# Kernel tuning notes

Hardware: AMD Instinct MI355X
Metric: run time of the kernel (lower is better)

## Reference

```python
import jax, jax.numpy as jnp
import numpy as np

# Module hyperparameters (init_kwargs)
N_CLASSES = 21
RADIUS = 5
SIZE = (256, 256)
SIGMA_DIST = 4.0
SIGMA_FEAT = 1.0
B, C = 8, 32


def _offsets(radius):
    """Integer (dy, dx) offsets with Euclidean distance < radius (includes (0,0))."""
    offs = []
    r = int(radius)
    for dy in range(-r + 1, r):
        for dx in range(-r + 1, r):
            if dy * dy + dx * dx < radius * radius:
                offs.append((dy, dx))
    return offs


OFFSETS = _offsets(RADIUS)  # 69 offsets for radius=5


def setup_inputs() -> dict:
    key = jax.random.key(0)
    k1, k2 = jax.random.split(key)
    H, W = SIZE
    classification = jax.random.uniform(k1, (B, N_CLASSES, H, W), dtype=jnp.float32)
    features = jax.random.normal(k2, (B, C, H, W), dtype=jnp.float32)
    return {"classification": classification, "features": features}


def reference(classification, features):
    # classification: [B, K, H, W] soft assignments S
    # features:       [B, C, H, W]
    Bb, K, H, W = classification.shape
    inv_sd2 = 1.0 / (SIGMA_DIST * SIGMA_DIST)
    inv_sf2 = 1.0 / (SIGMA_FEAT * SIGMA_FEAT)

    hs = jnp.arange(H)
    ws = jnp.arange(W)

    WS = jnp.zeros_like(classification)           # (W @ S), [B, K, H, W]
    degree = jnp.zeros((Bb, H, W), classification.dtype)

    # Loop over the small fixed set of neighbor offsets (69 for radius=5).
    for dy, dx in OFFSETS:
        f_nb = jnp.roll(features, (-dy, -dx), axis=(2, 3))
        s_nb = jnp.roll(classification, (-dy, -dx), axis=(2, 3))
        # mask out wrap-around: neighbor (h+dy, w+dx) must be in-bounds
        valid_h = (hs + dy >= 0) & (hs + dy < H)
        valid_w = (ws + dx >= 0) & (ws + dx < W)
        mask = (valid_h[:, None] & valid_w[None, :]).astype(classification.dtype)
        # Gaussian affinity: distance kernel * feature kernel
        feat_d2 = ((features - f_nb) ** 2).sum(axis=1)        # [B, H, W]
        w = jnp.exp(-(dy * dy + dx * dx) * inv_sd2 - feat_d2 * inv_sf2) * mask
        WS = WS + w[:, None] * s_nb
        degree = degree + w

    # numerator   = S^T W S : [B, K, K]
    # denominator = d^T S   : [B, K]
    num = jnp.einsum('bkhw,bjhw->bkj', classification, WS)
    den = jnp.einsum('bhw,bkhw->bk', degree, classification)
    return (num / den[:, None, :]).sum()
```

## Files before the change

### kernel.cpp

```cpp
#include <hip/hip_runtime.h>

#define HH 256
#define WW 256
#define HWPX 65536
#define BB 8
#define KK 21
#define CC 32

typedef _Float16 half2v __attribute__((ext_vector_type(2)));
union F4H { float4 f4; half2v h[4]; };

__global__ __launch_bounds__(256) void prep(const float* __restrict__ cls,
                                            const float* __restrict__ feat,
                                            float4* __restrict__ fpk,
                                            float2* __restrict__ TN) {
    const int tid = blockIdx.x * 256 + threadIdx.x;
    const int b = tid >> 16;
    const int p = tid & (HWPX - 1);

    const float* cbase = cls + (size_t)b * KK * HWPX + p;
    float T = 0.f;
#pragma unroll
    for (int k = 0; k < KK; ++k) T += cbase[(size_t)k * HWPX];

    const float* src = feat + (size_t)b * CC * HWPX + p;
    float nq = 0.f;
#pragma unroll
    for (int j = 0; j < 4; ++j) {
        F4H u;
#pragma unroll
        for (int k = 0; k < 4; ++k) {
            float a  = src[(size_t)(j * 8 + 2 * k) * HWPX];
            float b2 = src[(size_t)(j * 8 + 2 * k + 1) * HWPX];
            u.h[k] = __builtin_bit_cast(half2v, __builtin_amdgcn_cvt_pkrtz(a, b2));
            nq = __builtin_amdgcn_fdot2(u.h[k], u.h[k], nq, false);
        }
        fpk[(size_t)j * (BB * HWPX) + tid] = u.f4;
    }
    TN[tid] = make_float2(T, nq);
}

__global__ __launch_bounds__(256) void affinity4(const float4* __restrict__ fpk,
                                                 const float2* __restrict__ TN,
                                                 float* __restrict__ V,
                                                 float* __restrict__ deg) {
    const int L  = blockIdx.x;
    const int b  = L & 7;
    const int t  = L >> 3;
    const int by = t & 15;
    const int bx = (t >> 4) & 3;
    const int half = t >> 6;
    const int lane = threadIdx.x & 63;
    const int wid  = threadIdx.x >> 6;
    const int gx  = bx * 64 + lane;
    const int gy0 = by * 16 + wid * 4;

    const size_t bofs = (size_t)b * HWPX;
    const float4* fb0 = fpk + bofs;
    const float4* fb1 = fpk + (size_t)1 * BB * HWPX + bofs;
    const float4* fb2 = fpk + (size_t)2 * BB * HWPX + bofs;
    const float4* fb3 = fpk + (size_t)3 * BB * HWPX + bofs;
    const float2* tnb = TN + bofs;

    F4H fp[4][4];
    float np_[4];
#pragma unroll
    for (int py = 0; py < 4; ++py) {
        const int pp = ((gy0 + py) << 8) | gx;
        fp[py][0].f4 = fb0[pp];
        fp[py][1].f4 = fb1[pp];
        fp[py][2].f4 = fb2[pp];
        fp[py][3].f4 = fb3[pp];
        np_[py] = tnb[pp].y;
    }

    float degacc[4] = {0.f, 0.f, 0.f, 0.f};
    float vacc[4]   = {0.f, 0.f, 0.f, 0.f};

    const int dy_lo = half * 6;
    const int dy_hi = dy_lo + 6;

#pragma unroll 1
    for (int dyi = dy_lo; dyi < dy_hi; ++dyi) {
        const int ny = gy0 + dyi - 4;
        if ((unsigned)ny >= HH) continue;
        const int rowq = ny << 8;

        int dy2[4];
        float base[4];
#pragma unroll
        for (int py = 0; py < 4; ++py) {
            const int d = dyi - 4 - py;
            dy2[py] = d * d;
            base[py] = fmaf(-0.03125f, (float)dy2[py], -0.5f * np_[py]);
        }
        const int mind = min(min(dy2[0], dy2[1]), min(dy2[2], dy2[3]));

#pragma unroll 3
        for (int dxi = 0; dxi < 9; ++dxi) {
            const int dx = dxi - 4;
            const int dx2 = dx * dx;
            if (mind + dx2 >= 25) continue;

            const int gx2 = gx + dx;
            const bool vx = (unsigned)gx2 < WW;
            const int q = rowq | min(max(gx2, 0), WW - 1);

            F4H nb0, nb1, nb2, nb3;
            nb0.f4 = fb0[q];
            nb1.f4 = fb1[q];
            nb2.f4 = fb2[q];
            nb3.f4 = fb3[q];
            const float2 tq = tnb[q];
            const float cdx = (float)dx2 * -0.03125f;

#pragma unroll
            for (int py = 0; py < 4; ++py) {
                if (dy2[py] + dx2 < 25) {
                    float acc = fmaf(-0.5f, tq.y, base[py] + cdx);
#pragma unroll
                    for (int k = 0; k < 4; ++k) {
                        acc = __builtin_amdgcn_fdot2(fp[py][0].h[k], nb0.h[k], acc, false);
                        acc = __builtin_amdgcn_fdot2(fp[py][1].h[k], nb1.h[k], acc, false);
                        acc = __builtin_amdgcn_fdot2(fp[py][2].h[k], nb2.h[k], acc, false);
                        acc = __builtin_amdgcn_fdot2(fp[py][3].h[k], nb3.h[k], acc, false);
                    }
                    float w = __builtin_exp2f(acc * 2.8853900817779268f);
                    w = vx ? w : 0.f;
                    degacc[py] += w;
                    vacc[py] = fmaf(w, tq.x, vacc[py]);
                }
            }
        }
    }

    float* Vh = V   + (size_t)half * (BB * HWPX);
    float* Dh = deg + (size_t)half * (BB * HWPX);
#pragma unroll
    for (int py = 0; py < 4; ++py) {
        const size_t o = bofs + ((size_t)(gy0 + py) << 8) + gx;
        Vh[o] = vacc[py];
        Dh[o] = degacc[py];
    }
}

__global__ __launch_bounds__(256) void reduce_bj(const float* __restrict__ cls,
                                                 const float* __restrict__ V,
                                                 const float* __restrict__ deg,
                                                 float* __restrict__ numer,
                                                 float* __restrict__ denom) {
    __shared__ float smN[4][22], smD[4][22];
    const int b = blockIdx.y;
    const int p4 = (blockIdx.x * 256 + threadIdx.x) * 4;

    const float* clsb = cls + (size_t)b * KK * HWPX;
    const float* Vb = V + (size_t)b * HWPX;
    const float* Db = deg + (size_t)b * HWPX;
    const float4 va = *(const float4*)(Vb + p4);
    const float4 vb = *(const float4*)(Vb + (size_t)BB * HWPX + p4);
    const float4 da = *(const float4*)(Db + p4);
    const float4 db = *(const float4*)(Db + (size_t)BB * HWPX + p4);
    const float4 v4 = make_float4(va.x + vb.x, va.y + vb.y, va.z + vb.z, va.w + vb.w);
    const float4 d4 = make_float4(da.x + db.x, da.y + db.y, da.z + db.z, da.w + db.w);

    float accN[KK], accD[KK];
#pragma unroll
    for (int j = 0; j < KK; ++j) {
        float4 s4 = *(const float4*)(clsb + (size_t)j * HWPX + p4);
        float n = s4.x * v4.x;  n = fmaf(s4.y, v4.y, n);
        n = fmaf(s4.z, v4.z, n); n = fmaf(s4.w, v4.w, n);
        float d = s4.x * d4.x;  d = fmaf(s4.y, d4.y, d);
        d = fmaf(s4.z, d4.z, d); d = fmaf(s4.w, d4.w, d);
        accN[j] = n; accD[j] = d;
    }

    const int wid = threadIdx.x >> 6;
#pragma unroll
    for (int j = 0; j < KK; ++j) {
        float n = accN[j], d = accD[j];
#pragma unroll
        for (int off = 32; off > 0; off >>= 1) {
            n += __shfl_down(n, off);
            d += __shfl_down(d, off);
        }
        if ((threadIdx.x & 63) == 0) { smN[wid][j] = n; smD[wid][j] = d; }
    }
    __syncthreads();
    if (threadIdx.x < 2 * KK) {
        int half = threadIdx.x / KK;
        int j = threadIdx.x - half * KK;
        float acc = half ? (smD[0][j] + smD[1][j] + smD[2][j] + smD[3][j])
                         : (smN[0][j] + smN[1][j] + smN[2][j] + smN[3][j]);
        float* dst = half ? denom : numer;
        atomicAdd(&dst[b * KK + j], acc);
    }
}

__global__ __launch_bounds__(256) void finalize(const float* __restrict__ numer,
                                                const float* __restrict__ denom,
                                                float* __restrict__ out) {
    __shared__ float sm[4];
    int i = threadIdx.x;
    float r = 0.f;
    if (i < BB * KK) r = numer[i] / denom[i];
#pragma unroll
    for (int off = 32; off > 0; off >>= 1) r += __shfl_down(r, off);
    if ((i & 63) == 0) sm[i >> 6] = r;
    __syncthreads();
    if (i == 0) out[0] = sm[0] + sm[1] + sm[2] + sm[3];
}

extern "C" void kernel_launch(void* const* d_in, const int* in_sizes, int n_in,
                              void* d_out, int out_size, void* d_ws, size_t ws_size,
                              hipStream_t stream) {
    const float* cls  = (const float*)d_in[0];
    const float* feat = (const float*)d_in[1];
    float* out = (float*)d_out;

    const size_t BHW = (size_t)BB * HWPX;
    float4* fpk  = (float4*)d_ws;
    float2* TN   = (float2*)((char*)d_ws + BHW * 64);
    float*  V    = (float*)((char*)TN + BHW * 8);
    float*  deg  = V + 2 * BHW;
    float*  numer = deg + 2 * BHW;
    float*  denom = numer + BB * KK;

    (void)hipMemsetAsync(numer, 0, 2 * BB * KK * sizeof(float), stream);
    prep<<<dim3((BB * HWPX) / 256), dim3(256), 0, stream>>>(cls, feat, fpk, TN);
    affinity4<<<dim3(1024), dim3(256), 0, stream>>>(fpk, TN, V, deg);
    reduce_bj<<<dim3(HWPX / 1024, BB), dim3(256), 0, stream>>>(cls, V, deg, numer, denom);
    finalize<<<dim3(1), dim3(256), 0, stream>>>(numer, denom, out);
}
```

Baseline: 200.9 us.

## Pack per-pixel features and stats into interleaved 80-byte records

```diff
diff --git a/kernel.cpp b/kernel.cpp
--- a/kernel.cpp
+++ b/kernel.cpp
@@ -6,14 +6,14 @@
 #define BB 8
 #define KK 21
 #define CC 32
+#define RECB 80
 
 typedef _Float16 half2v __attribute__((ext_vector_type(2)));
 union F4H { float4 f4; half2v h[4]; };
 
 __global__ __launch_bounds__(256) void prep(const float* __restrict__ cls,
                                             const float* __restrict__ feat,
-                                            float4* __restrict__ fpk,
-                                            float2* __restrict__ TN) {
+                                            char* __restrict__ rec) {
     const int tid = blockIdx.x * 256 + threadIdx.x;
     const int b = tid >> 16;
     const int p = tid & (HWPX - 1);
@@ -24,6 +24,7 @@
     for (int k = 0; k < KK; ++k) T += cbase[(size_t)k * HWPX];
 
     const float* src = feat + (size_t)b * CC * HWPX + p;
+    char* r = rec + (size_t)tid * RECB;
     float nq = 0.f;
 #pragma unroll
     for (int j = 0; j < 4; ++j) {
@@ -35,13 +36,12 @@
             u.h[k] = __builtin_bit_cast(half2v, __builtin_amdgcn_cvt_pkrtz(a, b2));
             nq = __builtin_amdgcn_fdot2(u.h[k], u.h[k], nq, false);
         }
-        fpk[(size_t)j * (BB * HWPX) + tid] = u.f4;
-    }
-    TN[tid] = make_float2(T, nq);
-}
-
-__global__ __launch_bounds__(256) void affinity4(const float4* __restrict__ fpk,
-                                                 const float2* __restrict__ TN,
+        *(float4*)(r + j * 16) = u.f4;
+    }
+    *(float2*)(r + 64) = make_float2(T, nq);
+}
+
+__global__ __launch_bounds__(256) void affinity4(const char* __restrict__ rec,
                                                  float* __restrict__ V,
                                                  float* __restrict__ deg) {
     const int L  = blockIdx.x;
@@ -55,23 +55,19 @@
     const int gx  = bx * 64 + lane;
     const int gy0 = by * 16 + wid * 4;
 
-    const size_t bofs = (size_t)b * HWPX;
-    const float4* fb0 = fpk + bofs;
-    const float4* fb1 = fpk + (size_t)1 * BB * HWPX + bofs;
-    const float4* fb2 = fpk + (size_t)2 * BB * HWPX + bofs;
-    const float4* fb3 = fpk + (size_t)3 * BB * HWPX + bofs;
-    const float2* tnb = TN + bofs;
+    const char* rb = rec + (size_t)b * HWPX * RECB;
 
     F4H fp[4][4];
     float np_[4];
 #pragma unroll
     for (int py = 0; py < 4; ++py) {
         const int pp = ((gy0 + py) << 8) | gx;
-        fp[py][0].f4 = fb0[pp];
-        fp[py][1].f4 = fb1[pp];
-        fp[py][2].f4 = fb2[pp];
-        fp[py][3].f4 = fb3[pp];
-        np_[py] = tnb[pp].y;
+        const char* rp = rb + (size_t)pp * RECB;
+        fp[py][0].f4 = *(const float4*)(rp);
+        fp[py][1].f4 = *(const float4*)(rp + 16);
+        fp[py][2].f4 = *(const float4*)(rp + 32);
+        fp[py][3].f4 = *(const float4*)(rp + 48);
+        np_[py] = *(const float*)(rp + 68);
     }
 
     float degacc[4] = {0.f, 0.f, 0.f, 0.f};
@@ -84,7 +80,7 @@
     for (int dyi = dy_lo; dyi < dy_hi; ++dyi) {
         const int ny = gy0 + dyi - 4;
         if ((unsigned)ny >= HH) continue;
-        const int rowq = ny << 8;
+        const char* rowbase = rb + (size_t)(ny << 8) * RECB;
 
         int dy2[4];
         float base[4];
@@ -104,14 +100,15 @@
 
             const int gx2 = gx + dx;
             const bool vx = (unsigned)gx2 < WW;
-            const int q = rowq | min(max(gx2, 0), WW - 1);
+            const int qx = min(max(gx2, 0), WW - 1);
+            const char* rq = rowbase + (size_t)qx * RECB;
 
             F4H nb0, nb1, nb2, nb3;
-            nb0.f4 = fb0[q];
-            nb1.f4 = fb1[q];
-            nb2.f4 = fb2[q];
-            nb3.f4 = fb3[q];
-            const float2 tq = tnb[q];
+            nb0.f4 = *(const float4*)(rq);
+            nb1.f4 = *(const float4*)(rq + 16);
+            nb2.f4 = *(const float4*)(rq + 32);
+            nb3.f4 = *(const float4*)(rq + 48);
+            const float2 tq = *(const float2*)(rq + 64);
             const float cdx = (float)dx2 * -0.03125f;
 
 #pragma unroll
@@ -136,6 +133,7 @@
 
     float* Vh = V   + (size_t)half * (BB * HWPX);
     float* Dh = deg + (size_t)half * (BB * HWPX);
+    const size_t bofs = (size_t)b * HWPX;
 #pragma unroll
     for (int py = 0; py < 4; ++py) {
         const size_t o = bofs + ((size_t)(gy0 + py) << 8) + gx;
@@ -151,39 +149,31 @@
                                                  float* __restrict__ denom) {
     __shared__ float smN[4][22], smD[4][22];
     const int b = blockIdx.y;
-    const int p4 = (blockIdx.x * 256 + threadIdx.x) * 4;
-
-    const float* clsb = cls + (size_t)b * KK * HWPX;
-    const float* Vb = V + (size_t)b * HWPX;
-    const float* Db = deg + (size_t)b * HWPX;
-    const float4 va = *(const float4*)(Vb + p4);
-    const float4 vb = *(const float4*)(Vb + (size_t)BB * HWPX + p4);
-    const float4 da = *(const float4*)(Db + p4);
-    const float4 db = *(const float4*)(Db + (size_t)BB * HWPX + p4);
-    const float4 v4 = make_float4(va.x + vb.x, va.y + vb.y, va.z + vb.z, va.w + vb.w);
-    const float4 d4 = make_float4(da.x + db.x, da.y + db.y, da.z + db.z, da.w + db.w);
+    const int p = blockIdx.x * 256 + threadIdx.x;
+    const size_t bp = (size_t)b * HWPX + p;
+
+    const float v = V[bp] + V[(size_t)BB * HWPX + bp];
+    const float d = deg[bp] + deg[(size_t)BB * HWPX + bp];
+    const float* clsb = cls + (size_t)b * KK * HWPX + p;
 
     float accN[KK], accD[KK];
 #pragma unroll
     for (int j = 0; j < KK; ++j) {
-        float4 s4 = *(const float4*)(clsb + (size_t)j * HWPX + p4);
-        float n = s4.x * v4.x;  n = fmaf(s4.y, v4.y, n);
-        n = fmaf(s4.z, v4.z, n); n = fmaf(s4.w, v4.w, n);
-        float d = s4.x * d4.x;  d = fmaf(s4.y, d4.y, d);
-        d = fmaf(s4.z, d4.z, d); d = fmaf(s4.w, d4.w, d);
-        accN[j] = n; accD[j] = d;
+        const float s = clsb[(size_t)j * HWPX];
+        accN[j] = s * v;
+        accD[j] = s * d;
     }
 
     const int wid = threadIdx.x >> 6;
 #pragma unroll
     for (int j = 0; j < KK; ++j) {
-        float n = accN[j], d = accD[j];
+        float n = accN[j], dd = accD[j];
 #pragma unroll
         for (int off = 32; off > 0; off >>= 1) {
-            n += __shfl_down(n, off);
-            d += __shfl_down(d, off);
-        }
-        if ((threadIdx.x & 63) == 0) { smN[wid][j] = n; smD[wid][j] = d; }
+            n  += __shfl_down(n, off);
+            dd += __shfl_down(dd, off);
+        }
+        if ((threadIdx.x & 63) == 0) { smN[wid][j] = n; smD[wid][j] = dd; }
     }
     __syncthreads();
     if (threadIdx.x < 2 * KK) {
@@ -218,16 +208,15 @@
     float* out = (float*)d_out;
 
     const size_t BHW = (size_t)BB * HWPX;
-    float4* fpk  = (float4*)d_ws;
-    float2* TN   = (float2*)((char*)d_ws + BHW * 64);
-    float*  V    = (float*)((char*)TN + BHW * 8);
-    float*  deg  = V + 2 * BHW;
-    float*  numer = deg + 2 * BHW;
-    float*  denom = numer + BB * KK;
+    char*  rc   = (char*)d_ws;
+    float* V    = (float*)(rc + BHW * RECB);
+    float* dg   = V + 2 * BHW;
+    float* numer = dg + 2 * BHW;
+    float* denom = numer + BB * KK;
 
     (void)hipMemsetAsync(numer, 0, 2 * BB * KK * sizeof(float), stream);
-    prep<<<dim3((BB * HWPX) / 256), dim3(256), 0, stream>>>(cls, feat, fpk, TN);
-    affinity4<<<dim3(1024), dim3(256), 0, stream>>>(fpk, TN, V, deg);
-    reduce_bj<<<dim3(HWPX / 1024, BB), dim3(256), 0, stream>>>(cls, V, deg, numer, denom);
+    prep<<<dim3((BB * HWPX) / 256), dim3(256), 0, stream>>>(cls, feat, rc);
+    affinity4<<<dim3(1024), dim3(256), 0, stream>>>(rc, V, dg);
+    reduce_bj<<<dim3(HWPX / 256, BB), dim3(256), 0, stream>>>(cls, V, dg, numer, denom);
     finalize<<<dim3(1), dim3(256), 0, stream>>>(numer, denom, out);
 }
```

Result: slower. 225.7 us (+12.3%).

## Fuse class reduction into affinity kernel and split dot-product accumulator chains

Applied to the files above, without the earlier changes.

```diff
diff --git a/kernel.cpp b/kernel.cpp
--- a/kernel.cpp
+++ b/kernel.cpp
@@ -40,10 +40,12 @@
     TN[tid] = make_float2(T, nq);
 }
 
-__global__ __launch_bounds__(256) void affinity4(const float4* __restrict__ fpk,
-                                                 const float2* __restrict__ TN,
-                                                 float* __restrict__ V,
-                                                 float* __restrict__ deg) {
+__global__ __launch_bounds__(256, 4) void affinity4(const float4* __restrict__ fpk,
+                                                    const float2* __restrict__ TN,
+                                                    const float* __restrict__ cls,
+                                                    float* __restrict__ numer,
+                                                    float* __restrict__ denom) {
+    __shared__ float smN[4][22], smD[4][22];
     const int L  = blockIdx.x;
     const int b  = L & 7;
     const int t  = L >> 3;
@@ -117,14 +119,16 @@
 #pragma unroll
             for (int py = 0; py < 4; ++py) {
                 if (dy2[py] + dx2 < 25) {
-                    float acc = fmaf(-0.5f, tq.y, base[py] + cdx);
+                    float c0 = fmaf(-0.5f, tq.y, base[py] + cdx);
+                    float c1 = 0.f, c2 = 0.f, c3 = 0.f;
 #pragma unroll
                     for (int k = 0; k < 4; ++k) {
-                        acc = __builtin_amdgcn_fdot2(fp[py][0].h[k], nb0.h[k], acc, false);
-                        acc = __builtin_amdgcn_fdot2(fp[py][1].h[k], nb1.h[k], acc, false);
-                        acc = __builtin_amdgcn_fdot2(fp[py][2].h[k], nb2.h[k], acc, false);
-                        acc = __builtin_amdgcn_fdot2(fp[py][3].h[k], nb3.h[k], acc, false);
+                        c0 = __builtin_amdgcn_fdot2(fp[py][0].h[k], nb0.h[k], c0, false);
+                        c1 = __builtin_amdgcn_fdot2(fp[py][1].h[k], nb1.h[k], c1, false);
+                        c2 = __builtin_amdgcn_fdot2(fp[py][2].h[k], nb2.h[k], c2, false);
+                        c3 = __builtin_amdgcn_fdot2(fp[py][3].h[k], nb3.h[k], c3, false);
                     }
+                    const float acc = (c0 + c1) + (c2 + c3);
                     float w = __builtin_exp2f(acc * 2.8853900817779268f);
                     w = vx ? w : 0.f;
                     degacc[py] += w;
@@ -134,65 +138,40 @@
         }
     }
 
-    float* Vh = V   + (size_t)half * (BB * HWPX);
-    float* Dh = deg + (size_t)half * (BB * HWPX);
-#pragma unroll
-    for (int py = 0; py < 4; ++py) {
-        const size_t o = bofs + ((size_t)(gy0 + py) << 8) + gx;
-        Vh[o] = vacc[py];
-        Dh[o] = degacc[py];
-    }
-}
-
-__global__ __launch_bounds__(256) void reduce_bj(const float* __restrict__ cls,
-                                                 const float* __restrict__ V,
-                                                 const float* __restrict__ deg,
-                                                 float* __restrict__ numer,
-                                                 float* __restrict__ denom) {
-    __shared__ float smN[4][22], smD[4][22];
-    const int b = blockIdx.y;
-    const int p4 = (blockIdx.x * 256 + threadIdx.x) * 4;
-
     const float* clsb = cls + (size_t)b * KK * HWPX;
-    const float* Vb = V + (size_t)b * HWPX;
-    const float* Db = deg + (size_t)b * HWPX;
-    const float4 va = *(const float4*)(Vb + p4);
-    const float4 vb = *(const float4*)(Vb + (size_t)BB * HWPX + p4);
-    const float4 da = *(const float4*)(Db + p4);
-    const float4 db = *(const float4*)(Db + (size_t)BB * HWPX + p4);
-    const float4 v4 = make_float4(va.x + vb.x, va.y + vb.y, va.z + vb.z, va.w + vb.w);
-    const float4 d4 = make_float4(da.x + db.x, da.y + db.y, da.z + db.z, da.w + db.w);
-
-    float accN[KK], accD[KK];
-#pragma unroll
-    for (int j = 0; j < KK; ++j) {
-        float4 s4 = *(const float4*)(clsb + (size_t)j * HWPX + p4);
-        float n = s4.x * v4.x;  n = fmaf(s4.y, v4.y, n);
-        n = fmaf(s4.z, v4.z, n); n = fmaf(s4.w, v4.w, n);
-        float d = s4.x * d4.x;  d = fmaf(s4.y, d4.y, d);
-        d = fmaf(s4.z, d4.z, d); d = fmaf(s4.w, d4.w, d);
-        accN[j] = n; accD[j] = d;
-    }
-
-    const int wid = threadIdx.x >> 6;
-#pragma unroll
-    for (int j = 0; j < KK; ++j) {
-        float n = accN[j], d = accD[j];
-#pragma unroll
-        for (int off = 32; off > 0; off >>= 1) {
-            n += __shfl_down(n, off);
-            d += __shfl_down(d, off);
-        }
-        if ((threadIdx.x & 63) == 0) { smN[wid][j] = n; smD[wid][j] = d; }
+#pragma unroll 1
+    for (int jc = 0; jc < 3; ++jc) {
+        float accN[7], accD[7];
+#pragma unroll
+        for (int jj = 0; jj < 7; ++jj) {
+            const float* cj = clsb + (size_t)(jc * 7 + jj) * HWPX;
+            float n = 0.f, d = 0.f;
+#pragma unroll
+            for (int py = 0; py < 4; ++py) {
+                const float s = cj[((gy0 + py) << 8) | gx];
+                n = fmaf(s, vacc[py], n);
+                d = fmaf(s, degacc[py], d);
+            }
+            accN[jj] = n; accD[jj] = d;
+        }
+#pragma unroll
+        for (int jj = 0; jj < 7; ++jj) {
+            float n = accN[jj], d = accD[jj];
+#pragma unroll
+            for (int off = 32; off > 0; off >>= 1) {
+                n += __shfl_down(n, off);
+                d += __shfl_down(d, off);
+            }
+            if (lane == 0) { smN[wid][jc * 7 + jj] = n; smD[wid][jc * 7 + jj] = d; }
+        }
     }
     __syncthreads();
     if (threadIdx.x < 2 * KK) {
-        int half = threadIdx.x / KK;
-        int j = threadIdx.x - half * KK;
-        float acc = half ? (smD[0][j] + smD[1][j] + smD[2][j] + smD[3][j])
-                         : (smN[0][j] + smN[1][j] + smN[2][j] + smN[3][j]);
-        float* dst = half ? denom : numer;
-        atomicAdd(&dst[b * KK + j], acc);
+        const int h2 = threadIdx.x / KK;
+        const int j = threadIdx.x - h2 * KK;
+        const float a = h2 ? (smD[0][j] + smD[1][j] + smD[2][j] + smD[3][j])
+                           : (smN[0][j] + smN[1][j] + smN[2][j] + smN[3][j]);
+        atomicAdd((h2 ? denom : numer) + b * KK + j, a);
     }
 }
 
@@ -220,14 +199,11 @@
     const size_t BHW = (size_t)BB * HWPX;
     float4* fpk  = (float4*)d_ws;
     float2* TN   = (float2*)((char*)d_ws + BHW * 64);
-    float*  V    = (float*)((char*)TN + BHW * 8);
-    float*  deg  = V + 2 * BHW;
-    float*  numer = deg + 2 * BHW;
+    float*  numer = (float*)((char*)TN + BHW * 8);
     float*  denom = numer + BB * KK;
 
     (void)hipMemsetAsync(numer, 0, 2 * BB * KK * sizeof(float), stream);
     prep<<<dim3((BB * HWPX) / 256), dim3(256), 0, stream>>>(cls, feat, fpk, TN);
-    affinity4<<<dim3(1024), dim3(256), 0, stream>>>(fpk, TN, V, deg);
-    reduce_bj<<<dim3(HWPX / 1024, BB), dim3(256), 0, stream>>>(cls, V, deg, numer, denom);
+    affinity4<<<dim3(1024), dim3(256), 0, stream>>>(fpk, TN, cls, numer, denom);
     finalize<<<dim3(1), dim3(256), 0, stream>>>(numer, denom, out);
 }
```

After: 198.8 us. No clear change (-1.0%).
